# Kernel optimization log

Hardware: AMD Instinct MI355X
Metric: run time of the kernel (lower is better)

Reference implementation:

```python
import jax, jax.numpy as jnp
import numpy as np

B, N, F, H, K, HID, TAB = 4, 256, 1024, 16, 128, 4096, 32
D = F // H
PI = 3.14159  # matches literal in source


def setup_inputs() -> dict:
    key = jax.random.key(0)
    ks = jax.random.split(key, 20)
    r = lambda i, shape: jax.random.normal(ks[i], shape, jnp.float32) * 0.02
    return dict(
        nfeat=jax.random.normal(ks[0], (B, N, F), jnp.float32),
        sp_dist=jax.random.randint(ks[1], (B, N, N), 0, TAB, dtype=jnp.int32),
        rd_dist=jax.random.uniform(ks[2], (B, N, N), jnp.float32),
        dist_table=r(3, (TAB, K)),
        g_means=jax.random.uniform(ks[4], (K,), jnp.float32, 0.0, 3.0),
        g_stds=jax.random.uniform(ks[5], (K,), jnp.float32, 0.0, 3.0),
        g_mul=jnp.ones((1,), jnp.float32),
        g_bias=jnp.zeros((1,), jnp.float32),
        mlp_w1=r(6, (2 * K, H)), mlp_b1=jnp.zeros((H,), jnp.float32),
        mlp_w2=r(7, (H, H)), mlp_b2=jnp.zeros((H,), jnp.float32),
        wq=r(8, (F, F)), bq=jnp.zeros((F,), jnp.float32),
        wk=r(9, (F, F)), bk=jnp.zeros((F,), jnp.float32),
        wv=r(10, (F, F)), bv=jnp.zeros((F,), jnp.float32),
        wo=r(11, (F, F)), bo=jnp.zeros((F,), jnp.float32),
        ffn_w1=r(12, (F, HID)), ffn_b1=jnp.zeros((HID,), jnp.float32),
        ffn_w2=r(13, (HID, F)), ffn_b2=jnp.zeros((F,), jnp.float32),
        ln1_g=jnp.ones((F,), jnp.float32), ln1_b=jnp.zeros((F,), jnp.float32),
        ln2_g=jnp.ones((F,), jnp.float32), ln2_b=jnp.zeros((F,), jnp.float32),
    )


def _layer_norm(x, g, b):
    m = x.mean(-1, keepdims=True)
    v = ((x - m) ** 2).mean(-1, keepdims=True)
    return (x - m) / jnp.sqrt(v + 1e-5) * g + b


def reference(nfeat, sp_dist, rd_dist, dist_table, g_means, g_stds, g_mul, g_bias,
              mlp_w1, mlp_b1, mlp_w2, mlp_b2, wq, bq, wk, bk, wv, bv, wo, bo,
              ffn_w1, ffn_b1, ffn_w2, ffn_b2, ln1_g, ln1_b, ln2_g, ln2_b):
    # --- FusedDistEncoder: shortest-path embedding + Gaussian resistance-distance encoding ---
    sp_emb = dist_table[sp_dist]                      # [B,N,N,K]
    x = g_mul * rd_dist[..., None] + g_bias           # [B,N,N,1] -> broadcast over K
    std = jnp.abs(g_stds) + 0.01                      # [K]
    rd_emb = jnp.exp(-0.5 * ((x - g_means) / std) ** 2) / (((2 * PI) ** 0.5) * std)
    h = jnp.concatenate([sp_emb, rd_emb], axis=-1)    # [B,N,N,2K]
    h = jax.nn.gelu(h @ mlp_w1 + mlp_b1, approximate=False)
    attn_bias = h @ mlp_w2 + mlp_b2                   # [B,N,N,H]

    # --- BiasedMultiheadAttention (note: source divides q by scaling=d^-0.5, i.e. *sqrt(d)) ---
    q = (nfeat @ wq + bq).reshape(B, N, H, D) * (D ** 0.5)
    k = (nfeat @ wk + bk).reshape(B, N, H, D)
    v = (nfeat @ wv + bv).reshape(B, N, H, D)
    scores = jnp.einsum('bihd,bjhd->bijh', q, k) + attn_bias   # [B,N,N,H]
    w = jax.nn.softmax(scores, axis=2)                          # softmax over key dim j
    attn = jnp.einsum('bijh,bjhd->bihd', w, v).reshape(B, N, F) @ wo + bo

    # --- GraphormerLayer residuals (post-norm, dropout=0 / eval) ---
    x1 = _layer_norm(nfeat + attn, ln1_g, ln1_b)
    ffn = jax.nn.relu(x1 @ ffn_w1 + ffn_b1) @ ffn_w2 + ffn_b2
    return _layer_norm(x1 + ffn, ln2_g, ln2_b)
```

## Files before the change

kernel.cpp:

```cpp
#include <hip/hip_runtime.h>
#include <hip/hip_bf16.h>
#include <math.h>

typedef __hip_bfloat16 bf16;
typedef float f32x4 __attribute__((ext_vector_type(4)));
typedef short bf16x8 __attribute__((ext_vector_type(8)));

#define AS1 __attribute__((address_space(1)))
#define AS3 __attribute__((address_space(3)))

#define ASM_VMCNT4 asm volatile("s_waitcnt vmcnt(4)" ::: "memory")
#define ASM_VMCNT0 asm volatile("s_waitcnt vmcnt(0)" ::: "memory")
#define ASM_LGKM0  asm volatile("s_waitcnt lgkmcnt(0)" ::: "memory")
#define ASM_BARRIER asm volatile("s_barrier" ::: "memory")

__global__ __launch_bounds__(256) void setup_kernel(
    const float* __restrict__ nfeat, bf16* __restrict__ nfeatb,
    const float* __restrict__ bq, const float* __restrict__ bk,
    const float* __restrict__ bv, float* __restrict__ bqkv,
    const float* __restrict__ table, const float* __restrict__ w1,
    float* __restrict__ tw)
{
    int bid = blockIdx.x, t = threadIdx.x;
    if (bid < 1024) {
        int i = (bid * 256 + t) * 4;
        float4 v = *reinterpret_cast<const float4*>(nfeat + i);
        nfeatb[i + 0] = (bf16)v.x; nfeatb[i + 1] = (bf16)v.y;
        nfeatb[i + 2] = (bf16)v.z; nfeatb[i + 3] = (bf16)v.w;
    } else if (bid < 1036) {
        int i = (bid - 1024) * 256 + t;
        bqkv[i] = i < 1024 ? bq[i] : (i < 2048 ? bk[i - 1024] : bv[i - 2048]);
    } else {
        #pragma unroll
        for (int e = t; e < 512; e += 256) {
            int r = e >> 4, o = e & 15;
            float a = 0.f;
            for (int k = 0; k < 128; ++k) a += table[r * 128 + k] * w1[k * 16 + o];
            tw[e] = a;
        }
    }
}

__global__ __launch_bounds__(256) void wtx_kernel(
    const float* __restrict__ wq, const float* __restrict__ wk,
    const float* __restrict__ wv, const float* __restrict__ wo,
    const float* __restrict__ fw1, const float* __restrict__ fw2,
    bf16* __restrict__ qkvT, bf16* __restrict__ woT,
    bf16* __restrict__ fw1T, bf16* __restrict__ fw2T)
{
    __shared__ float tile[64][68];
    int bid = blockIdx.x, t = threadIdx.x;
    const float* W; bf16* WT; int Kd, Nd, local;
    if (bid < 768)       { int ws = bid >> 8; local = bid & 255;
                           W = ws == 0 ? wq : ws == 1 ? wk : wv;
                           WT = qkvT + ws * 1048576; Kd = 1024; Nd = 1024; }
    else if (bid < 1024) { local = bid - 768;  W = wo;  WT = woT;  Kd = 1024; Nd = 1024; }
    else if (bid < 2048) { local = bid - 1024; W = fw1; WT = fw1T; Kd = 1024; Nd = 4096; }
    else                 { local = bid - 2048; W = fw2; WT = fw2T; Kd = 4096; Nd = 1024; }
    int ntn = Nd >> 6;
    int k0 = (local / ntn) * 64, n0 = (local % ntn) * 64;

    {
        int k = t >> 2, nb = (t & 3) * 16;
        const float* src = W + (size_t)(k0 + k) * Nd + n0 + nb;
        #pragma unroll
        for (int c = 0; c < 4; c++) {
            float4 v = *reinterpret_cast<const float4*>(src + c * 4);
            *reinterpret_cast<float4*>(&tile[k][nb + c * 4]) = v;
        }
    }
    __syncthreads();

    {
        int w = t >> 6, l = t & 63;
        int n = w * 16 + (l >> 2), kb = (l & 3) * 16;
        bf16x8 o0, o1;
        #pragma unroll
        for (int j = 0; j < 8; j++) {
            union { bf16 b; short s; } u;
            u.b = (bf16)tile[kb + j][n];
            o0[j] = u.s;
        }
        #pragma unroll
        for (int j = 0; j < 8; j++) {
            union { bf16 b; short s; } u;
            u.b = (bf16)tile[kb + 8 + j][n];
            o1[j] = u.s;
        }
        bf16* dst = WT + (size_t)(n0 + n) * Kd + k0 + kb;
        *reinterpret_cast<bf16x8*>(dst) = o0;
        *reinterpret_cast<bf16x8*>(dst + 8) = o1;
    }
}

__global__ __launch_bounds__(256) void enc_kernel(
    const int* __restrict__ sp, const float* __restrict__ rd,
    const float* __restrict__ tw,
    const float* __restrict__ means, const float* __restrict__ stds,
    const float* __restrict__ gmul, const float* __restrict__ gbias,
    const float* __restrict__ w1, const float* __restrict__ b1,
    const float* __restrict__ w2, const float* __restrict__ b2,
    bf16* __restrict__ biasT)
{
    __shared__ float w1s[128][16];
    __shared__ float w2s[16][16];
    __shared__ float b1s[16], b2s[16];
    __shared__ float meanS[128], istdS[128], coefS[128];
    int t = threadIdx.x;
    for (int i = t; i < 2048; i += 256) w1s[i >> 4][i & 15] = w1[2048 + i];
    w2s[t >> 4][t & 15] = w2[t];
    if (t < 16) { b1s[t] = b1[t]; b2s[t] = b2[t]; }
    if (t < 128) {
        float s = fabsf(stds[t]) + 0.01f;
        meanS[t] = means[t];
        istdS[t] = 1.f / s;
        coefS[t] = 1.f / (sqrtf(2.f * 3.14159f) * s);
    }
    __syncthreads();

    int p = blockIdx.x * 256 + t;
    int idx = sp[p];
    float xv = gmul[0] * rd[p] + gbias[0];

    float acc[16];
    #pragma unroll
    for (int o = 0; o < 16; o++) acc[o] = b1s[o] + tw[idx * 16 + o];

    for (int k = 0; k < 128; k++) {
        float d = (xv - meanS[k]) * istdS[k];
        float g = coefS[k] * __expf(-0.5f * d * d);
        #pragma unroll
        for (int o = 0; o < 16; o++) acc[o] += g * w1s[k][o];
    }
    float h[16];
    #pragma unroll
    for (int o = 0; o < 16; o++) {
        float a = acc[o];
        h[o] = 0.5f * a * (1.f + erff(a * 0.70710678118f));
    }
    float outv[16];
    #pragma unroll
    for (int o = 0; o < 16; o++) outv[o] = b2s[o];
    #pragma unroll
    for (int q = 0; q < 16; q++) {
        float hq = h[q];
        #pragma unroll
        for (int o = 0; o < 16; o++) outv[o] += hq * w2s[q][o];
    }
    int b = blockIdx.x >> 8, i = blockIdx.x & 255;
    #pragma unroll
    for (int hh = 0; hh < 16; hh++)
        biasT[(((b * 16 + hh) * 256 + i) << 8) + t] = (bf16)outv[hh];
}

__global__ __launch_bounds__(256, 3) void gemm_bf16(
    const bf16* __restrict__ A, const bf16* __restrict__ BT,
    const float* __restrict__ bias, const float* __restrict__ add,
    void* __restrict__ C, int M, int Nd, int Kd, int epi)
{
    __shared__ __align__(16) char smem[49152];
    int t = threadIdx.x;
    int w = t >> 6, l = t & 63;
    int wr = w >> 1, wc = w & 1;
    int lr = l & 15, hi = l >> 4;
    int row0 = blockIdx.y * 64, col0 = blockIdx.x * 64;
    int nz = gridDim.z;
    int klen = Kd / nz;
    int kbeg = blockIdx.z * klen;

    f32x4 acc[2][2];
    #pragma unroll
    for (int i = 0; i < 2; i++)
        #pragma unroll
        for (int j = 0; j < 2; j++) acc[i][j] = (f32x4){0.f, 0.f, 0.f, 0.f};

    const bf16* Asrc = A + (row0 + (t & 63)) * Kd + kbeg + (t >> 6) * 8;
    const bf16* Bsrc = BT + (col0 + (t & 63)) * Kd + kbeg + (t >> 6) * 8;
    int wbase = (t & 192) * 16;

    #pragma unroll
    for (int p = 0; p < 2; p++) {
        __builtin_amdgcn_global_load_lds((const AS1 void*)(Asrc + p * 32),
                                         (AS3 void*)(smem + p * 4096 + wbase), 16, 0, 0);
        __builtin_amdgcn_global_load_lds((const AS1 void*)(Bsrc + p * 32),
                                         (AS3 void*)(smem + 8192 + p * 4096 + wbase), 16, 0, 0);
    }
    #pragma unroll
    for (int p = 0; p < 2; p++) {
        __builtin_amdgcn_global_load_lds((const AS1 void*)(Asrc + 64 + p * 32),
                                         (AS3 void*)(smem + 16384 + p * 4096 + wbase), 16, 0, 0);
        __builtin_amdgcn_global_load_lds((const AS1 void*)(Bsrc + 64 + p * 32),
                                         (AS3 void*)(smem + 16384 + 8192 + p * 4096 + wbase), 16, 0, 0);
    }

    int nsteps = klen >> 6;
    int cur = 0;
    for (int s = 0; s < nsteps; ++s) {
        if (s + 1 < nsteps) { ASM_VMCNT4; }
        else               { ASM_VMCNT0; }
        ASM_BARRIER;

        if (s + 2 < nsteps) {
            const bf16* An = Asrc + (s + 2) * 64;
            const bf16* Bn = Bsrc + (s + 2) * 64;
            int nb = cur + 2; if (nb >= 3) nb -= 3;
            char* dst = smem + nb * 16384;
            #pragma unroll
            for (int p = 0; p < 2; p++) {
                __builtin_amdgcn_global_load_lds((const AS1 void*)(An + p * 32),
                    (AS3 void*)(dst + p * 4096 + wbase), 16, 0, 0);
                __builtin_amdgcn_global_load_lds((const AS1 void*)(Bn + p * 32),
                    (AS3 void*)(dst + 8192 + p * 4096 + wbase), 16, 0, 0);
            }
        }

        const char* base = smem + cur * 16384;
        bf16x8 af[2][2], bfr[2][2];
        #pragma unroll
        for (int kk = 0; kk < 2; kk++) {
            #pragma unroll
            for (int mi = 0; mi < 2; mi++)
                af[kk][mi] = *(const bf16x8*)(base + kk * 4096 + hi * 1024 +
                                              (wr * 32 + mi * 16 + lr) * 16);
            #pragma unroll
            for (int nj = 0; nj < 2; nj++)
                bfr[kk][nj] = *(const bf16x8*)(base + 8192 + kk * 4096 + hi * 1024 +
                                               (wc * 32 + nj * 16 + lr) * 16);
        }
        ASM_LGKM0;
        __builtin_amdgcn_sched_barrier(0);
        __builtin_amdgcn_s_setprio(1);
        #pragma unroll
        for (int kk = 0; kk < 2; kk++)
            #pragma unroll
            for (int mi = 0; mi < 2; mi++)
                #pragma unroll
                for (int nj = 0; nj < 2; nj++)
                    acc[mi][nj] = __builtin_amdgcn_mfma_f32_16x16x32_bf16(
                        af[kk][mi], bfr[kk][nj], acc[mi][nj], 0, 0, 0);
        __builtin_amdgcn_s_setprio(0);
        cur = cur + 1; if (cur >= 3) cur = 0;
    }

    if (nz > 1) {
        float* P = (float*)C + (size_t)blockIdx.z * M * Nd;
        #pragma unroll
        for (int i = 0; i < 2; i++) {
            int rb = row0 + wr * 32 + i * 16 + hi * 4;
            #pragma unroll
            for (int j = 0; j < 2; j++) {
                int cc = col0 + wc * 32 + j * 16 + lr;
                f32x4 v = acc[i][j];
                #pragma unroll
                for (int q = 0; q < 4; q++) P[(rb + q) * Nd + cc] = v[q];
            }
        }
        return;
    }

    #pragma unroll
    for (int i = 0; i < 2; i++) {
        int rb = row0 + wr * 32 + i * 16 + hi * 4;
        #pragma unroll
        for (int j = 0; j < 2; j++) {
            int cc = col0 + wc * 32 + j * 16 + lr;
            float bsv = bias[cc];
            f32x4 v = acc[i][j];
            #pragma unroll
            for (int q = 0; q < 4; q++) {
                int r = rb + q;
                float x = v[q] + bsv;
                if (epi == 0) {
                    ((float*)C)[r * Nd + cc] = x;
                } else if (epi == 1) {
                    ((float*)C)[r * Nd + cc] = x + add[r * Nd + cc];
                } else if (epi == 2) {
                    ((bf16*)C)[r * Nd + cc] = (bf16)fmaxf(x, 0.f);
                } else {
                    bf16* Cb = (bf16*)C;
                    int sel = cc >> 10, ccc = cc & 1023;
                    int hh = ccc >> 6, dd = ccc & 63;
                    int bb = r >> 8, ii = r & 255;
                    if (sel == 0)
                        Cb[(((bb * 16 + hh) * 256 + ii) << 6) + dd] = (bf16)(x * 8.0f);
                    else if (sel == 1)
                        Cb[1048576 + (((bb * 16 + hh) * 256 + ii) << 6) + dd] = (bf16)x;
                    else
                        Cb[2097152 + ((((bb * 16 + hh) << 6) + dd) << 8) + ii] = (bf16)x;
                }
            }
        }
    }
}

__global__ __launch_bounds__(256) void flash_kernel(
    const bf16* __restrict__ Qb, const bf16* __restrict__ Kb,
    const bf16* __restrict__ VT, const bf16* __restrict__ biasT,
    bf16* __restrict__ out)
{
    __shared__ __align__(16) char pls[32768];
    int t = threadIdx.x;
    int w = t >> 6, l = t & 63;
    int lr = l & 15, hi = l >> 4;
    int bh = blockIdx.x >> 2, iq = blockIdx.x & 3;
    int b = bh >> 4, h = bh & 15;
    int i0 = iq * 64 + w * 16;

    const bf16* Qp = Qb + (bh * 256 + i0 + lr) * 64 + hi * 8;
    bf16x8 qf0 = *(const bf16x8*)(Qp);
    bf16x8 qf1 = *(const bf16x8*)(Qp + 32);

    f32x4 acc[16];
    #pragma unroll
    for (int f = 0; f < 16; f++) acc[f] = (f32x4){0.f, 0.f, 0.f, 0.f};

    const bf16* Kp = Kb + (bh * 256 + lr) * 64 + hi * 8;
    #pragma unroll
    for (int f = 0; f < 16; f++) {
        bf16x8 kf0 = *(const bf16x8*)(Kp + f * 1024);
        bf16x8 kf1 = *(const bf16x8*)(Kp + f * 1024 + 32);
        acc[f] = __builtin_amdgcn_mfma_f32_16x16x32_bf16(qf0, kf0, acc[f], 0, 0, 0);
        acc[f] = __builtin_amdgcn_mfma_f32_16x16x32_bf16(qf1, kf1, acc[f], 0, 0, 0);
    }

    const bf16* bp = biasT + (bh * 256 + i0 + hi * 4) * 256 + lr;
    #pragma unroll
    for (int f = 0; f < 16; f++)
        #pragma unroll
        for (int q = 0; q < 4; q++)
            acc[f][q] += __bfloat162float(bp[q * 256 + f * 16]);

    float inv[4];
    #pragma unroll
    for (int q = 0; q < 4; q++) {
        float m = acc[0][q];
        #pragma unroll
        for (int f = 1; f < 16; f++) m = fmaxf(m, acc[f][q]);
        #pragma unroll
        for (int msk = 1; msk < 16; msk <<= 1) m = fmaxf(m, __shfl_xor(m, msk));
        float s = 0.f;
        #pragma unroll
        for (int f = 0; f < 16; f++) {
            float e = __expf(acc[f][q] - m);
            acc[f][q] = e;
            s += e;
        }
        #pragma unroll
        for (int msk = 1; msk < 16; msk <<= 1) s += __shfl_xor(s, msk);
        inv[q] = 1.f / s;
    }

    char* Pw = pls + w * 8192;
    #pragma unroll
    for (int f = 0; f < 16; f++) {
        int j = f * 16 + lr;
        int c = j >> 3, jo = j & 7;
        #pragma unroll
        for (int q = 0; q < 4; q++)
            *(bf16*)(Pw + c * 256 + (hi * 4 + q) * 16 + jo * 2) = (bf16)(acc[f][q] * inv[q]);
    }
    __syncthreads();

    const char* Pr = pls + w * 8192 + hi * 256 + lr * 16;
    const bf16* Vp = VT + (bh * 64 + lr) * 256 + hi * 8;
    #pragma unroll
    for (int n = 0; n < 4; n++) {
        f32x4 o = (f32x4){0.f, 0.f, 0.f, 0.f};
        #pragma unroll
        for (int ks = 0; ks < 8; ks++) {
            bf16x8 pa = *(const bf16x8*)(Pr + ks * 1024);
            bf16x8 vb = *(const bf16x8*)(Vp + n * 4096 + ks * 32);
            o = __builtin_amdgcn_mfma_f32_16x16x32_bf16(pa, vb, o, 0, 0, 0);
        }
        #pragma unroll
        for (int q = 0; q < 4; q++)
            out[(b * 256 + i0 + hi * 4 + q) * 1024 + h * 64 + n * 16 + lr] = (bf16)o[q];
    }
}

__global__ __launch_bounds__(256) void ln_fused_kernel(
    const float* __restrict__ part, int S,
    const float* __restrict__ bias, const float* __restrict__ add,
    const float* __restrict__ g, const float* __restrict__ bta,
    float* __restrict__ out, bf16* __restrict__ ob)
{
    int row = blockIdx.x;
    int t = threadIdx.x;
    float v[4];
    float sum = 0.f;
    #pragma unroll
    for (int i = 0; i < 4; i++) {
        int c = t + i * 256;
        float x = add[row * 1024 + c] + bias[c];
        for (int s = 0; s < S; s++) x += part[s * 1048576 + row * 1024 + c];
        v[i] = x;
        sum += x;
    }
    __shared__ float red[8];
    #pragma unroll
    for (int off = 32; off; off >>= 1) sum += __shfl_xor(sum, off);
    if ((t & 63) == 0) red[t >> 6] = sum;
    __syncthreads();
    float mean = (red[0] + red[1] + red[2] + red[3]) * (1.f / 1024.f);
    float vs = 0.f;
    #pragma unroll
    for (int i = 0; i < 4; i++) { float d = v[i] - mean; vs += d * d; }
    #pragma unroll
    for (int off = 32; off; off >>= 1) vs += __shfl_xor(vs, off);
    if ((t & 63) == 0) red[4 + (t >> 6)] = vs;
    __syncthreads();
    float var = (red[4] + red[5] + red[6] + red[7]) * (1.f / 1024.f);
    float invs = rsqrtf(var + 1e-5f);
    #pragma unroll
    for (int i = 0; i < 4; i++) {
        int c = t + i * 256;
        float o = (v[i] - mean) * invs * g[c] + bta[c];
        out[row * 1024 + c] = o;
        if (ob) ob[row * 1024 + c] = (bf16)o;
    }
}

extern "C" void kernel_launch(void* const* d_in, const int* in_sizes, int n_in,
                              void* d_out, int out_size, void* d_ws, size_t ws_size,
                              hipStream_t stream)
{
    const float* nfeat  = (const float*)d_in[0];
    const int*   sp     = (const int*)  d_in[1];
    const float* rd     = (const float*)d_in[2];
    const float* table  = (const float*)d_in[3];
    const float* gmeans = (const float*)d_in[4];
    const float* gstds  = (const float*)d_in[5];
    const float* gmul   = (const float*)d_in[6];
    const float* gbias  = (const float*)d_in[7];
    const float* w1     = (const float*)d_in[8];
    const float* b1     = (const float*)d_in[9];
    const float* w2     = (const float*)d_in[10];
    const float* b2     = (const float*)d_in[11];
    const float* wq     = (const float*)d_in[12];
    const float* bq     = (const float*)d_in[13];
    const float* wk     = (const float*)d_in[14];
    const float* bk     = (const float*)d_in[15];
    const float* wv     = (const float*)d_in[16];
    const float* bv     = (const float*)d_in[17];
    const float* wo     = (const float*)d_in[18];
    const float* bo     = (const float*)d_in[19];
    const float* fw1    = (const float*)d_in[20];
    const float* fb1    = (const float*)d_in[21];
    const float* fw2    = (const float*)d_in[22];
    const float* fb2    = (const float*)d_in[23];
    const float* ln1g   = (const float*)d_in[24];
    const float* ln1b   = (const float*)d_in[25];
    const float* ln2g   = (const float*)d_in[26];
    const float* ln2b   = (const float*)d_in[27];

    const size_t MB = 1 << 20;
    char* cws = (char*)d_ws;
    bf16*  biasT   = (bf16*)(cws);
    bf16*  qkvb    = (bf16*)(cws + 8 * MB);
    float* part    = (float*)(cws + 8 * MB);
    bf16*  qkvT    = (bf16*)(cws + 16 * MB);
    bf16*  woT     = (bf16*)(cws + 22 * MB);
    bf16*  fw1T    = (bf16*)(cws + 24 * MB);
    bf16*  fw2T    = (bf16*)(cws + 32 * MB);
    float* x1      = (float*)(cws + 40 * MB);
    bf16*  nfeatb  = (bf16*)(cws + 44 * MB);
    bf16*  x1b     = (bf16*)(cws + 46 * MB);
    bf16*  attnob  = (bf16*)(cws + 48 * MB);
    float* bqkv    = (float*)(cws + 50 * MB);
    float* tw      = (float*)(cws + 50 * MB + 16384);
    bf16*  hiddenb = biasT;

    setup_kernel<<<1037, 256, 0, stream>>>(nfeat, nfeatb, bq, bk, bv, bqkv,
                                           table, w1, tw);
    wtx_kernel<<<3072, 256, 0, stream>>>(wq, wk, wv, wo, fw1, fw2,
                                         qkvT, woT, fw1T, fw2T);
    enc_kernel<<<1024, 256, 0, stream>>>(sp, rd, tw, gmeans, gstds, gmul, gbias,
                                         w1, b1, w2, b2, biasT);

    gemm_bf16<<<dim3(48, 16), 256, 0, stream>>>(nfeatb, qkvT, bqkv, nullptr, qkvb,
                                                1024, 3072, 1024, 3);

    flash_kernel<<<256, 256, 0, stream>>>(qkvb, qkvb + 1048576, qkvb + 2097152,
                                          biasT, attnob);

    gemm_bf16<<<dim3(16, 16, 2), 256, 0, stream>>>(attnob, woT, bo, nullptr, part,
                                                   1024, 1024, 1024, 0);
    ln_fused_kernel<<<1024, 256, 0, stream>>>(part, 2, bo, nfeat, ln1g, ln1b, x1, x1b);

    gemm_bf16<<<dim3(64, 16), 256, 0, stream>>>(x1b, fw1T, fb1, nullptr, hiddenb,
                                                1024, 4096, 1024, 2);

    gemm_bf16<<<dim3(16, 16, 4), 256, 0, stream>>>(hiddenb, fw2T, fb2, nullptr, part,
                                                   1024, 1024, 4096, 0);
    ln_fused_kernel<<<1024, 256, 0, stream>>>(part, 4, fb2, x1, ln2g, ln2b,
                                              (float*)d_out, nullptr);
}
```

Measured before the change: 192.8 us.

## Add single-wave 32x32 split-K GEMM for the output and FFN2 projections

Adds a new one-wavefront kernel that computes 32x32 tiles with split-K partials and uses it for the Wo and FFN-down projections. The 1024-column GEMMs previously ran as 64x64 tiles with split-K of 2 or 4. They now run as 4096 small blocks, with split-K 4 for Wo, to fill more CUs on the chip. Split-K handling is removed from the original kernel, and the workspace is remapped to hold the larger fp32 partial buffer. The trade-off is more partial-sum traffic and reduction work in the layer-norm kernel, plus less data reuse per block.

```diff
diff --git a/kernel.cpp b/kernel.cpp
--- a/kernel.cpp
+++ b/kernel.cpp
@@ -153,10 +153,10 @@
         biasT[(((b * 16 + hh) * 256 + i) << 8) + t] = (bf16)outv[hh];
 }
 
-__global__ __launch_bounds__(256, 3) void gemm_bf16(
+__global__ __launch_bounds__(256, 3) void kgemm(
     const bf16* __restrict__ A, const bf16* __restrict__ BT,
-    const float* __restrict__ bias, const float* __restrict__ add,
-    void* __restrict__ C, int M, int Nd, int Kd, int epi)
+    const float* __restrict__ bias, void* __restrict__ C,
+    int M, int Nd, int Kd, int epi)
 {
     __shared__ __align__(16) char smem[49152];
     int t = threadIdx.x;
@@ -164,9 +164,6 @@
     int wr = w >> 1, wc = w & 1;
     int lr = l & 15, hi = l >> 4;
     int row0 = blockIdx.y * 64, col0 = blockIdx.x * 64;
-    int nz = gridDim.z;
-    int klen = Kd / nz;
-    int kbeg = blockIdx.z * klen;
 
     f32x4 acc[2][2];
     #pragma unroll
@@ -174,8 +171,8 @@
         #pragma unroll
         for (int j = 0; j < 2; j++) acc[i][j] = (f32x4){0.f, 0.f, 0.f, 0.f};
 
-    const bf16* Asrc = A + (row0 + (t & 63)) * Kd + kbeg + (t >> 6) * 8;
-    const bf16* Bsrc = BT + (col0 + (t & 63)) * Kd + kbeg + (t >> 6) * 8;
+    const bf16* Asrc = A + (size_t)(row0 + (t & 63)) * Kd + (t >> 6) * 8;
+    const bf16* Bsrc = BT + (size_t)(col0 + (t & 63)) * Kd + (t >> 6) * 8;
     int wbase = (t & 192) * 16;
 
     #pragma unroll
@@ -193,7 +190,7 @@
                                          (AS3 void*)(smem + 16384 + 8192 + p * 4096 + wbase), 16, 0, 0);
     }
 
-    int nsteps = klen >> 6;
+    int nsteps = Kd >> 6;
     int cur = 0;
     for (int s = 0; s < nsteps; ++s) {
         if (s + 1 < nsteps) { ASM_VMCNT4; }
@@ -242,22 +239,6 @@
         cur = cur + 1; if (cur >= 3) cur = 0;
     }
 
-    if (nz > 1) {
-        float* P = (float*)C + (size_t)blockIdx.z * M * Nd;
-        #pragma unroll
-        for (int i = 0; i < 2; i++) {
-            int rb = row0 + wr * 32 + i * 16 + hi * 4;
-            #pragma unroll
-            for (int j = 0; j < 2; j++) {
-                int cc = col0 + wc * 32 + j * 16 + lr;
-                f32x4 v = acc[i][j];
-                #pragma unroll
-                for (int q = 0; q < 4; q++) P[(rb + q) * Nd + cc] = v[q];
-            }
-        }
-        return;
-    }
-
     #pragma unroll
     for (int i = 0; i < 2; i++) {
         int rb = row0 + wr * 32 + i * 16 + hi * 4;
@@ -270,12 +251,8 @@
             for (int q = 0; q < 4; q++) {
                 int r = rb + q;
                 float x = v[q] + bsv;
-                if (epi == 0) {
-                    ((float*)C)[r * Nd + cc] = x;
-                } else if (epi == 1) {
-                    ((float*)C)[r * Nd + cc] = x + add[r * Nd + cc];
-                } else if (epi == 2) {
-                    ((bf16*)C)[r * Nd + cc] = (bf16)fmaxf(x, 0.f);
+                if (epi == 2) {
+                    ((bf16*)C)[(size_t)r * Nd + cc] = (bf16)fmaxf(x, 0.f);
                 } else {
                     bf16* Cb = (bf16*)C;
                     int sel = cc >> 10, ccc = cc & 1023;
@@ -289,6 +266,76 @@
                         Cb[2097152 + ((((bb * 16 + hh) << 6) + dd) << 8) + ii] = (bf16)x;
                 }
             }
+        }
+    }
+}
+
+__global__ __launch_bounds__(64, 8) void wgemm(
+    const bf16* __restrict__ A, const bf16* __restrict__ BT,
+    float* __restrict__ P, int M, int Nd, int Kd)
+{
+    __shared__ __align__(16) char smem[8192];
+    int l = threadIdx.x;
+    int lr = l & 15, hi = l >> 4;
+    int row0 = blockIdx.y * 32, col0 = blockIdx.x * 32;
+    int klen = Kd / gridDim.z, kbeg = blockIdx.z * klen;
+
+    f32x4 acc[2][2];
+    #pragma unroll
+    for (int i = 0; i < 2; i++)
+        #pragma unroll
+        for (int j = 0; j < 2; j++) acc[i][j] = (f32x4){0.f, 0.f, 0.f, 0.f};
+
+    const bf16* Asrc = A + (size_t)(row0 + (l & 31)) * Kd + kbeg + (l >> 5) * 8;
+    const bf16* Bsrc = BT + (size_t)(col0 + (l & 31)) * Kd + kbeg + (l >> 5) * 8;
+
+    #define WSTAGE(ss, buf)                                                     \
+        _Pragma("unroll")                                                       \
+        for (int p = 0; p < 2; p++) {                                           \
+            __builtin_amdgcn_global_load_lds((const AS1 void*)(Asrc + (ss) * 32 + p * 16), \
+                (AS3 void*)(smem + (buf) * 4096 + p * 1024), 16, 0, 0);         \
+            __builtin_amdgcn_global_load_lds((const AS1 void*)(Bsrc + (ss) * 32 + p * 16), \
+                (AS3 void*)(smem + (buf) * 4096 + 2048 + p * 1024), 16, 0, 0);  \
+        }
+
+    WSTAGE(0, 0);
+    WSTAGE(1, 1);
+
+    int nsteps = klen >> 5;
+    for (int s = 0; s < nsteps; ++s) {
+        int bufc = s & 1;
+        if (s + 1 < nsteps) { ASM_VMCNT4; }
+        else               { ASM_VMCNT0; }
+        const char* bb = smem + bufc * 4096;
+        bf16x8 af[2], bfr[2];
+        #pragma unroll
+        for (int mi = 0; mi < 2; mi++)
+            af[mi] = *(const bf16x8*)(bb + (hi * 32 + mi * 16 + lr) * 16);
+        #pragma unroll
+        for (int nj = 0; nj < 2; nj++)
+            bfr[nj] = *(const bf16x8*)(bb + 2048 + (hi * 32 + nj * 16 + lr) * 16);
+        ASM_LGKM0;
+        __builtin_amdgcn_sched_barrier(0);
+        if (s + 2 < nsteps) { WSTAGE(s + 2, bufc); }
+        #pragma unroll
+        for (int mi = 0; mi < 2; mi++)
+            #pragma unroll
+            for (int nj = 0; nj < 2; nj++)
+                acc[mi][nj] = __builtin_amdgcn_mfma_f32_16x16x32_bf16(
+                    af[mi], bfr[nj], acc[mi][nj], 0, 0, 0);
+    }
+    #undef WSTAGE
+
+    float* Pz = P + (size_t)blockIdx.z * M * Nd;
+    #pragma unroll
+    for (int mi = 0; mi < 2; mi++) {
+        int rb = row0 + mi * 16 + hi * 4;
+        #pragma unroll
+        for (int nj = 0; nj < 2; nj++) {
+            int cc = col0 + nj * 16 + lr;
+            f32x4 v = acc[mi][nj];
+            #pragma unroll
+            for (int q = 0; q < 4; q++) Pz[(size_t)(rb + q) * Nd + cc] = v[q];
         }
     }
 }
@@ -457,17 +504,17 @@
     char* cws = (char*)d_ws;
     bf16*  biasT   = (bf16*)(cws);
     bf16*  qkvb    = (bf16*)(cws + 8 * MB);
-    float* part    = (float*)(cws + 8 * MB);
-    bf16*  qkvT    = (bf16*)(cws + 16 * MB);
-    bf16*  woT     = (bf16*)(cws + 22 * MB);
-    bf16*  fw1T    = (bf16*)(cws + 24 * MB);
-    bf16*  fw2T    = (bf16*)(cws + 32 * MB);
-    float* x1      = (float*)(cws + 40 * MB);
-    bf16*  nfeatb  = (bf16*)(cws + 44 * MB);
-    bf16*  x1b     = (bf16*)(cws + 46 * MB);
-    bf16*  attnob  = (bf16*)(cws + 48 * MB);
-    float* bqkv    = (float*)(cws + 50 * MB);
-    float* tw      = (float*)(cws + 50 * MB + 16384);
+    float* part    = (float*)(cws + 16 * MB);
+    bf16*  qkvT    = (bf16*)(cws + 48 * MB);
+    bf16*  woT     = (bf16*)(cws + 54 * MB);
+    bf16*  fw1T    = (bf16*)(cws + 56 * MB);
+    bf16*  fw2T    = (bf16*)(cws + 64 * MB);
+    float* x1      = (float*)(cws + 72 * MB);
+    bf16*  nfeatb  = (bf16*)(cws + 76 * MB);
+    bf16*  x1b     = (bf16*)(cws + 78 * MB);
+    bf16*  attnob  = (bf16*)(cws + 80 * MB);
+    float* bqkv    = (float*)(cws + 82 * MB);
+    float* tw      = (float*)(cws + 82 * MB + 16384);
     bf16*  hiddenb = biasT;
 
     setup_kernel<<<1037, 256, 0, stream>>>(nfeat, nfeatb, bq, bk, bv, bqkv,
@@ -477,21 +524,19 @@
     enc_kernel<<<1024, 256, 0, stream>>>(sp, rd, tw, gmeans, gstds, gmul, gbias,
                                          w1, b1, w2, b2, biasT);
 
-    gemm_bf16<<<dim3(48, 16), 256, 0, stream>>>(nfeatb, qkvT, bqkv, nullptr, qkvb,
-                                                1024, 3072, 1024, 3);
+    kgemm<<<dim3(48, 16), 256, 0, stream>>>(nfeatb, qkvT, bqkv, qkvb,
+                                            1024, 3072, 1024, 3);
 
     flash_kernel<<<256, 256, 0, stream>>>(qkvb, qkvb + 1048576, qkvb + 2097152,
                                           biasT, attnob);
 
-    gemm_bf16<<<dim3(16, 16, 2), 256, 0, stream>>>(attnob, woT, bo, nullptr, part,
-                                                   1024, 1024, 1024, 0);
-    ln_fused_kernel<<<1024, 256, 0, stream>>>(part, 2, bo, nfeat, ln1g, ln1b, x1, x1b);
-
-    gemm_bf16<<<dim3(64, 16), 256, 0, stream>>>(x1b, fw1T, fb1, nullptr, hiddenb,
-                                                1024, 4096, 1024, 2);
-
-    gemm_bf16<<<dim3(16, 16, 4), 256, 0, stream>>>(hiddenb, fw2T, fb2, nullptr, part,
-                                                   1024, 1024, 4096, 0);
+    wgemm<<<dim3(32, 32, 4), 64, 0, stream>>>(attnob, woT, part, 1024, 1024, 1024);
+    ln_fused_kernel<<<1024, 256, 0, stream>>>(part, 4, bo, nfeat, ln1g, ln1b, x1, x1b);
+
+    kgemm<<<dim3(64, 16), 256, 0, stream>>>(x1b, fw1T, fb1, hiddenb,
+                                            1024, 4096, 1024, 2);
+
+    wgemm<<<dim3(32, 32, 4), 64, 0, stream>>>(hiddenb, fw2T, part, 1024, 1024, 4096);
     ln_fused_kernel<<<1024, 256, 0, stream>>>(part, 4, fb2, x1, ln2g, ln2b,
                                               (float*)d_out, nullptr);
 }
```

Result: slower. 228.7 us (+18.6%).
